# Kernel tuning notes

Measured on AMD Instinct MI355X. Metric: run time of the kernel, lower is better.

Reference implementation:

```python
import jax, jax.numpy as jnp
import numpy as np

B, S, D, H = 4, 1024, 2048, 16
DH = D // H  # 128
THETA = 10000.0


def setup_inputs() -> dict:
    key = jax.random.key(0)
    k1, k2, k3 = jax.random.split(key, 3)
    std_qkv = np.sqrt(2.0 / (D + 3 * D)).astype(np.float32)
    std_out = np.sqrt(2.0 / (D + D)).astype(np.float32)
    x = jax.random.normal(k1, (B, S, D), jnp.float32)
    w_qkv = jax.random.normal(k2, (D, 3 * D), jnp.float32) * std_qkv
    w_out = jax.random.normal(k3, (D, D), jnp.float32) * std_out
    # matrix-based RoPE table: [max_seq, d_head//2, 2, 2]
    freqs = jnp.arange(S, dtype=jnp.float32)[:, None] / THETA ** (
        2.0 * jnp.arange(DH // 2, dtype=jnp.float32) / DH)[None, :]
    eye = jnp.array([[1.0, 0.0], [0.0, 1.0]], jnp.float32)
    rot = jnp.array([[0.0, -1.0], [1.0, 0.0]], jnp.float32)
    rope_matrix = (jnp.cos(freqs)[:, :, None, None] * eye
                   + jnp.sin(freqs)[:, :, None, None] * rot)
    token_positions = jnp.arange(S, dtype=jnp.int32)
    return {"x": x, "w_qkv": w_qkv, "w_out": w_out,
            "rope_matrix": rope_matrix, "token_positions": token_positions}


def _apply_rope(t, pe):
    # t: [B, H, S, DH]; pe: [S, DH//2, 2, 2] (gathered by token_positions)
    tr = t.reshape(*t.shape[:-1], DH // 2, 2)  # interleaved (even, odd) pairs
    out = jnp.einsum('bhski,skoi->bhsko', tr, pe)
    return out.reshape(t.shape)


def reference(x, w_qkv, w_out, rope_matrix, token_positions):
    qkv = jnp.einsum('bsd,df->bsf', x, w_qkv)          # [B,S,3D]
    q, k, v = jnp.split(qkv, 3, axis=-1)
    to_heads = lambda t: t.reshape(B, S, H, DH).transpose(0, 2, 1, 3)
    q, k, v = to_heads(q), to_heads(k), to_heads(v)    # [B,H,S,DH]
    pe = rope_matrix[token_positions]                  # [S, DH//2, 2, 2]
    q = _apply_rope(q, pe)
    k = _apply_rope(k, pe)
    scores = jnp.einsum('bhqd,bhkd->bhqk', q, k) / np.float32(np.sqrt(DH))
    causal = jnp.tril(jnp.ones((S, S), dtype=bool))
    scores = jnp.where(causal, scores, -jnp.inf)
    attn = jax.nn.softmax(scores, axis=-1)
    ctx = jnp.einsum('bhqk,bhkd->bhqd', attn, v)       # [B,H,S,DH]
    ctx = ctx.transpose(0, 2, 1, 3).reshape(B, S, D)
    return jnp.einsum('bsd,df->bsf', ctx, w_out)
```

## Files before the change

kernel.cpp:

```cpp
#include <hip/hip_runtime.h>
#include <hip/hip_bf16.h>
#include <math.h>

#define Bn 4
#define Sn 1024
#define Dn 2048
#define Hn 16
#define DHn 128
#define BS (Bn * Sn)
#define QKVC (3 * Dn)

typedef __attribute__((ext_vector_type(8))) short short8;
typedef __attribute__((ext_vector_type(4))) float float4v;

__device__ inline unsigned short f2bf(float x) {
  union { float f; unsigned int u; } v; v.f = x;
  unsigned int r = v.u + 0x7fffu + ((v.u >> 16) & 1u);
  return (unsigned short)(r >> 16);
}
__device__ inline float bf2f(unsigned short b) {
  union { unsigned int u; float f; } v; v.u = ((unsigned int)b) << 16;
  return v.f;
}

__device__ __forceinline__ void gload16(const unsigned short* g, unsigned short* l) {
  __builtin_amdgcn_global_load_lds(
      (const __attribute__((address_space(1))) unsigned int*)g,
      (__attribute__((address_space(3))) unsigned int*)l, 16, 0, 0);
}

__global__ __launch_bounds__(256) void cvt_f32_bf16(
    const float* __restrict__ in, unsigned short* __restrict__ out, int n8) {
  int id = blockIdx.x * 256 + threadIdx.x;
  if (id >= n8) return;
  const float4* p = reinterpret_cast<const float4*>(in) + 2 * (size_t)id;
  float4 a = p[0], b = p[1];
  short8 o;
  o[0] = (short)f2bf(a.x); o[1] = (short)f2bf(a.y);
  o[2] = (short)f2bf(a.z); o[3] = (short)f2bf(a.w);
  o[4] = (short)f2bf(b.x); o[5] = (short)f2bf(b.y);
  o[6] = (short)f2bf(b.z); o[7] = (short)f2bf(b.w);
  *reinterpret_cast<short8*>(out + 8 * (size_t)id) = o;
}

__global__ __launch_bounds__(256) void transpose_cvt(
    const float* __restrict__ w, unsigned short* __restrict__ wT, int K, int N) {
  __shared__ unsigned short t[64][72];
  const int c0 = blockIdx.x * 64;
  const int r0 = blockIdx.y * 64;
  const int tid = threadIdx.x;
  const int r = tid >> 2;
  const int cb = (tid & 3) * 16;
#pragma unroll
  for (int it = 0; it < 4; ++it) {
    float4 v = *reinterpret_cast<const float4*>(&w[(long)(r0 + r) * N + c0 + cb + 4 * it]);
    t[r][cb + 4 * it + 0] = f2bf(v.x);
    t[r][cb + 4 * it + 1] = f2bf(v.y);
    t[r][cb + 4 * it + 2] = f2bf(v.z);
    t[r][cb + 4 * it + 3] = f2bf(v.w);
  }
  __syncthreads();
  unsigned short o[16];
#pragma unroll
  for (int e = 0; e < 16; ++e) o[e] = t[cb + e][r];
  unsigned short* dst = &wT[(long)(c0 + r) * K + r0 + cb];
  *reinterpret_cast<short8*>(dst) = *reinterpret_cast<short8*>(&o[0]);
  *reinterpret_cast<short8*>(dst + 8) = *reinterpret_cast<short8*>(&o[8]);
}

#define AB8(buf, h) ((buf) * 16384 + (h) * 8192)
#define BB8(buf) (32768 + (buf) * 8192)

#define VMW(n)                                                                 \
  asm volatile("s_waitcnt vmcnt(" #n ")" ::: "memory");                        \
  __builtin_amdgcn_sched_barrier(0);

#define PHASE(BUF, MIH, STAGE_STMT, WAIT_STMT)                                 \
  {                                                                            \
    __builtin_amdgcn_sched_barrier(0);                                         \
    short8 afr[2][2];                                                          \
    _Pragma("unroll") for (int mi2 = 0; mi2 < 2; ++mi2) {                      \
      const int mrow = wr * 64 + ((MIH) * 2 + mi2) * 16;                       \
      const int hh = mrow >> 7;                                                \
      const int rl = (mrow & 127) + c;                                         \
      _Pragma("unroll") for (int ks = 0; ks < 2; ++ks)                         \
        afr[mi2][ks] = *(const short8*)(lds + AB8(BUF, 0) + hh * 8192 +        \
            rl * 64 + (((ks * 4 + g) ^ cg7) << 3));                            \
    }                                                                          \
    if ((MIH) == 0) {                                                          \
      _Pragma("unroll") for (int ni = 0; ni < 4; ++ni)                         \
        _Pragma("unroll") for (int ks = 0; ks < 2; ++ks)                       \
          bfr[ni][ks] = *(const short8*)(lds + BB8(BUF) +                      \
              (wc * 64 + ni * 16 + c) * 64 + (((ks * 4 + g) ^ cg7) << 3));     \
    }                                                                          \
    STAGE_STMT;                                                                \
    __builtin_amdgcn_sched_barrier(0);                                         \
    __builtin_amdgcn_s_barrier();                                              \
    asm volatile("s_waitcnt lgkmcnt(0)" ::: "memory");                         \
    __builtin_amdgcn_sched_barrier(0);                                         \
    __builtin_amdgcn_s_setprio(1);                                             \
    _Pragma("unroll") for (int mi2 = 0; mi2 < 2; ++mi2)                        \
      _Pragma("unroll") for (int ni = 0; ni < 4; ++ni)                         \
        _Pragma("unroll") for (int ks = 0; ks < 2; ++ks)                       \
          acc[(MIH) * 2 + mi2][ni] = __builtin_amdgcn_mfma_f32_16x16x32_bf16(  \
              afr[mi2][ks], bfr[ni][ks], acc[(MIH) * 2 + mi2][ni], 0, 0, 0);   \
    __builtin_amdgcn_s_setprio(0);                                             \
    WAIT_STMT                                                                  \
    __builtin_amdgcn_s_barrier();                                              \
  }

#define GEMM_MAIN_LOOP(A_, BT_, K_)                                            \
  STAGE(A_ + (long)m0 * K_, AB8(0, 0));                                        \
  STAGE(A_ + (long)(m0 + 128) * K_, AB8(0, 1));                                \
  STAGE(BT_ + (long)n0 * K_, BB8(0));                                          \
  STAGE(BT_ + (long)n0 * K_ + 64, BB8(1));                                     \
  VMW(2)                                                                       \
  __builtin_amdgcn_s_barrier();                                                \
  for (int it2 = 0; it2 < nt / 2 - 1; ++it2) {                                 \
    const long T1 = (long)(2 * it2 + 1) * 64;                                  \
    const long T2 = (long)(2 * it2 + 2) * 64;                                  \
    const long T3 = (long)(2 * it2 + 3) * 64;                                  \
    PHASE(0, 0, STAGE(A_ + (long)m0 * K_ + T1, AB8(1, 0)), )                   \
    PHASE(0, 1,                                                                \
          { STAGE(A_ + (long)(m0 + 128) * K_ + T1, AB8(1, 1));                 \
            STAGE(BT_ + (long)n0 * K_ + T2, BB8(0)); }, VMW(2))                \
    PHASE(1, 0, STAGE(A_ + (long)m0 * K_ + T2, AB8(0, 0)), )                   \
    PHASE(1, 1,                                                                \
          { STAGE(A_ + (long)(m0 + 128) * K_ + T2, AB8(0, 1));                 \
            STAGE(BT_ + (long)n0 * K_ + T3, BB8(1)); }, VMW(2))                \
  }                                                                            \
  {                                                                            \
    const long TL = (long)(nt - 1) * 64;                                       \
    PHASE(0, 0, STAGE(A_ + (long)m0 * K_ + TL, AB8(1, 0)), )                   \
    PHASE(0, 1, STAGE(A_ + (long)(m0 + 128) * K_ + TL, AB8(1, 1)), VMW(0))     \
    PHASE(1, 0, {}, )                                                          \
    PHASE(1, 1, {}, )                                                          \
  }

__global__ __launch_bounds__(512, 2) void gemm_qkv(
    const unsigned short* __restrict__ A, const unsigned short* __restrict__ BT,
    const float* __restrict__ rope, const int* __restrict__ tpos,
    unsigned short* __restrict__ qR, unsigned short* __restrict__ kR,
    unsigned short* __restrict__ vT, int K) {
  __shared__ unsigned short lds[49152];
  const int tid = threadIdx.x;
  const int wid = tid >> 6, lane = tid & 63;
  const int c = lane & 15, g = lane >> 4;
  const int wr = wid >> 1, wc = wid & 1;
  const int cg7 = c & 7;

  const int nwg = gridDim.x * gridDim.y;
  const int bid = blockIdx.y * gridDim.x + blockIdx.x;
  const int swz = (bid & 7) * (nwg >> 3) + (bid >> 3);
  const int m0 = (swz % gridDim.x) * 256, n0 = (swz / gridDim.x) * 128;

  const int nt = K >> 6;

  float4v acc[4][4];
#pragma unroll
  for (int i = 0; i < 4; ++i)
#pragma unroll
    for (int j = 0; j < 4; ++j) acc[i][j] = (float4v){0.f, 0.f, 0.f, 0.f};
  short8 bfr[4][2];

  auto STAGE = [&](const unsigned short* gbase, int sbase) {
#pragma unroll
    for (int j = 0; j < 2; ++j) {
      const int ch = j * 512 + tid;
      const int r = ch >> 3;
      const int wo = (ch & 7) ^ (r & 7);
      gload16(gbase + (long)r * K + wo * 8, lds + sbase + j * 4096 + wid * 512);
    }
  };

  GEMM_MAIN_LOOP(A, BT, K)

  const int type = n0 >> 11;
  const int h = (n0 & 2047) >> 7;
  const long bh = (long)((m0 >> 10) * Hn + h);
  const int s0 = m0 & 1023;

  if (type == 2) {
#pragma unroll
    for (int mi = 0; mi < 4; ++mi)
#pragma unroll
      for (int ni = 0; ni < 4; ++ni)
#pragma unroll
        for (int j = 0; j < 4; ++j) {
          const int mm = wr * 64 + mi * 16 + g * 4 + j;
          const int nn = wc * 64 + ni * 16 + c;
          lds[nn * 264 + mm] = f2bf(acc[mi][ni][j]);
        }
    __syncthreads();
    unsigned short* dst = vT + bh * (long)DHn * Sn + s0;
#pragma unroll
    for (int it = 0; it < 8; ++it) {
      const int cid = it * 512 + tid;
      const int d = cid >> 5;
      const int sl = (cid & 31) * 8;
      short8 v = *reinterpret_cast<const short8*>(lds + d * 264 + sl);
      *reinterpret_cast<short8*>(dst + (long)d * Sn + sl) = v;
    }
  } else {
#pragma unroll
    for (int mi = 0; mi < 4; ++mi)
#pragma unroll
      for (int ni = 0; ni < 4; ++ni)
#pragma unroll
        for (int j = 0; j < 4; ++j) {
          const int mm = wr * 64 + mi * 16 + g * 4 + j;
          const int nn = wc * 64 + ni * 16 + c;
          lds[mm * 136 + nn] = f2bf(acc[mi][ni][j]);
        }
    __syncthreads();
    unsigned short* dst = (type == 0 ? qR : kR) + (bh * Sn + s0) * DHn;
    const float qsc = (type == 0) ? 0.1275174213f : 1.0f;
#pragma unroll
    for (int it = 0; it < 8; ++it) {
      const int cid = it * 512 + tid;
      const int r = cid >> 4;
      const int colc = (cid & 15) * 8;
      union { short8 v; unsigned short u[8]; } iw, ow;
      iw.v = *reinterpret_cast<const short8*>(lds + r * 136 + colc);
      const int pos = tpos[s0 + r];
      const float4* pe = reinterpret_cast<const float4*>(rope) +
                         (long)pos * 64 + (colc >> 1);
#pragma unroll
      for (int p = 0; p < 4; ++p) {
        const float4 m2 = pe[p];
        const float xx = bf2f(iw.u[2 * p]), yy = bf2f(iw.u[2 * p + 1]);
        ow.u[2 * p]     = f2bf((m2.x * xx + m2.y * yy) * qsc);
        ow.u[2 * p + 1] = f2bf((m2.z * xx + m2.w * yy) * qsc);
      }
      *reinterpret_cast<short8*>(dst + (long)r * DHn + colc) = ow.v;
    }
  }
}

__global__ __launch_bounds__(512, 2) void gemm_out(
    const unsigned short* __restrict__ A, const unsigned short* __restrict__ BT,
    float* __restrict__ Cout, int N, int K) {
  __shared__ unsigned short lds[49152];
  const int tid = threadIdx.x;
  const int wid = tid >> 6, lane = tid & 63;
  const int c = lane & 15, g = lane >> 4;
  const int wr = wid >> 1, wc = wid & 1;
  const int cg7 = c & 7;

  const int nwg = gridDim.x * gridDim.y;
  const int bid = blockIdx.y * gridDim.x + blockIdx.x;
  const int swz = (bid & 7) * (nwg >> 3) + (bid >> 3);
  const int m0 = (swz % gridDim.x) * 256, n0 = (swz / gridDim.x) * 128;

  const int nt = K >> 6;

  float4v acc[4][4];
#pragma unroll
  for (int i = 0; i < 4; ++i)
#pragma unroll
    for (int j = 0; j < 4; ++j) acc[i][j] = (float4v){0.f, 0.f, 0.f, 0.f};
  short8 bfr[4][2];

  auto STAGE = [&](const unsigned short* gbase, int sbase) {
#pragma unroll
    for (int j = 0; j < 2; ++j) {
      const int ch = j * 512 + tid;
      const int r = ch >> 3;
      const int wo = (ch & 7) ^ (r & 7);
      gload16(gbase + (long)r * K + wo * 8, lds + sbase + j * 4096 + wid * 512);
    }
  };

  GEMM_MAIN_LOOP(A, BT, K)

#pragma unroll
  for (int mi = 0; mi < 4; ++mi)
#pragma unroll
    for (int ni = 0; ni < 4; ++ni)
#pragma unroll
      for (int j = 0; j < 4; ++j) {
        const int m = m0 + wr * 64 + mi * 16 + g * 4 + j;
        const int n = n0 + wc * 64 + ni * 16 + c;
        Cout[(long)m * N + n] = acc[mi][ni][j];
      }
}
#undef PHASE
#undef GEMM_MAIN_LOOP

__global__ __launch_bounds__(256, 2) void attn_mfma(
    const unsigned short* __restrict__ qR, const unsigned short* __restrict__ kR,
    const unsigned short* __restrict__ vTd, unsigned short* __restrict__ ctx) {
  __shared__ unsigned short lds[32768];
  __shared__ unsigned short Ps[4][16][72];
  const int qt = gridDim.x - 1 - blockIdx.x;
  const int h = blockIdx.y, b = blockIdx.z;
  const int tid = threadIdx.x, wid = tid >> 6, lane = tid & 63;
  const int c = lane & 15, g = lane >> 4, cg7 = c & 7;
  const long bh = (long)(b * Hn + h);
  const unsigned short* kbase = kR + bh * Sn * DHn;
  const unsigned short* vbase = vTd + bh * DHn * Sn;

  short8 qf[4];
  {
    const unsigned short* qrow = qR + (bh * Sn + qt * 64 + wid * 16 + c) * DHn;
#pragma unroll
    for (int kc = 0; kc < 4; ++kc)
      qf[kc] = *reinterpret_cast<const short8*>(qrow + kc * 32 + g * 8);
  }

  auto STAGE = [&](int kt, int buf) {
#pragma unroll
    for (int j = 0; j < 4; ++j) {
      const int ch = j * 256 + tid;
      const int r = ch >> 4, wd = ch & 15;
      const int ws = (wd & 8) | ((wd & 7) ^ (r & 7));
      gload16(kbase + (long)kt * 8192 + r * 128 + ws * 8,
              lds + buf * 8192 + j * 2048 + wid * 512);
    }
#pragma unroll
    for (int j = 0; j < 4; ++j) {
      const int ch = j * 256 + tid;
      const int d = ch >> 3, sw = ch & 7;
      gload16(vbase + (long)d * Sn + kt * 64 + ((sw ^ (d & 7)) << 3),
              lds + 16384 + buf * 8192 + j * 2048 + wid * 512);
    }
  };

  float m = -INFINITY, lsum = 0.f;
  float4v ot[8];
#pragma unroll
  for (int fd = 0; fd < 8; ++fd) ot[fd] = (float4v){0.f, 0.f, 0.f, 0.f};

  STAGE(0, 0);
  __syncthreads();
  int cur = 0;

  for (int kt = 0; kt <= qt; ++kt) {
    if (kt < qt) STAGE(kt + 1, cur ^ 1);

    float4v scv[4];
#pragma unroll
    for (int f = 0; f < 4; ++f) scv[f] = (float4v){0.f, 0.f, 0.f, 0.f};
    __builtin_amdgcn_s_setprio(1);
#pragma unroll
    for (int f = 0; f < 4; ++f)
#pragma unroll
      for (int kc = 0; kc < 4; ++kc) {
        const int wp = kc * 4 + g;
        const int ws = (wp & 8) | ((wp & 7) ^ cg7);
        short8 kf = *reinterpret_cast<const short8*>(
            lds + cur * 8192 + (f * 16 + c) * 128 + ws * 8);
        scv[f] = __builtin_amdgcn_mfma_f32_16x16x32_bf16(kf, qf[kc], scv[f], 0, 0, 0);
      }
    __builtin_amdgcn_s_setprio(0);

    if (kt == qt) {
      const int qloc = wid * 16 + c;
#pragma unroll
      for (int f = 0; f < 4; ++f)
#pragma unroll
        for (int j = 0; j < 4; ++j)
          if (f * 16 + g * 4 + j > qloc) scv[f][j] = -INFINITY;
    }

    float tmax = -INFINITY;
#pragma unroll
    for (int f = 0; f < 4; ++f)
#pragma unroll
      for (int j = 0; j < 4; ++j) tmax = fmaxf(tmax, scv[f][j]);
    tmax = fmaxf(tmax, __shfl_xor(tmax, 16));
    tmax = fmaxf(tmax, __shfl_xor(tmax, 32));

    float mnew, corr;
    if (__all(tmax <= m + 8.f)) {
      mnew = m; corr = 1.f;
    } else {
      mnew = fmaxf(m, tmax);
      corr = exp2f(m - mnew);
#pragma unroll
      for (int fd = 0; fd < 8; ++fd) ot[fd] *= corr;
    }
    float psum = 0.f;
#pragma unroll
    for (int f = 0; f < 4; ++f)
#pragma unroll
      for (int j = 0; j < 4; ++j) {
        scv[f][j] = exp2f(scv[f][j] - mnew);
        psum += scv[f][j];
      }
    psum += __shfl_xor(psum, 16);
    psum += __shfl_xor(psum, 32);
    lsum = lsum * corr + psum;
    m = mnew;

#pragma unroll
    for (int f = 0; f < 4; ++f) {
      unsigned int lo = (unsigned)f2bf(scv[f][0]) | ((unsigned)f2bf(scv[f][1]) << 16);
      unsigned int hi = (unsigned)f2bf(scv[f][2]) | ((unsigned)f2bf(scv[f][3]) << 16);
      uint2 pk; pk.x = lo; pk.y = hi;
      *reinterpret_cast<uint2*>(&Ps[wid][c][f * 16 + g * 4]) = pk;
    }

    short8 pf0 = *reinterpret_cast<const short8*>(&Ps[wid][c][g * 8]);
    short8 pf1 = *reinterpret_cast<const short8*>(&Ps[wid][c][32 + g * 8]);
    __builtin_amdgcn_s_setprio(1);
#pragma unroll
    for (int fd = 0; fd < 8; ++fd) {
      short8 vf0 = *reinterpret_cast<const short8*>(
          lds + 16384 + cur * 8192 + (fd * 16 + c) * 64 + ((g ^ cg7) << 3));
      short8 vf1 = *reinterpret_cast<const short8*>(
          lds + 16384 + cur * 8192 + (fd * 16 + c) * 64 + (((g + 4) ^ cg7) << 3));
      ot[fd] = __builtin_amdgcn_mfma_f32_16x16x32_bf16(vf0, pf0, ot[fd], 0, 0, 0);
      ot[fd] = __builtin_amdgcn_mfma_f32_16x16x32_bf16(vf1, pf1, ot[fd], 0, 0, 0);
    }
    __builtin_amdgcn_s_setprio(0);

    __syncthreads();
    cur ^= 1;
  }

  const float inv = 1.0f / lsum;
  unsigned short* orow = ctx + (long)(b * Sn + qt * 64 + wid * 16 + c) * Dn + h * DHn;
#pragma unroll
  for (int fd = 0; fd < 8; ++fd) {
    const int d = fd * 16 + g * 4;
    uint2 pk;
    pk.x = (unsigned)f2bf(ot[fd][0] * inv) | ((unsigned)f2bf(ot[fd][1] * inv) << 16);
    pk.y = (unsigned)f2bf(ot[fd][2] * inv) | ((unsigned)f2bf(ot[fd][3] * inv) << 16);
    *reinterpret_cast<uint2*>(orow + d) = pk;
  }
}

extern "C" void kernel_launch(void* const* d_in, const int* in_sizes, int n_in,
                              void* d_out, int out_size, void* d_ws, size_t ws_size,
                              hipStream_t stream) {
  const float* x     = (const float*)d_in[0];
  const float* w_qkv = (const float*)d_in[1];
  const float* w_out = (const float*)d_in[2];
  const float* rope  = (const float*)d_in[3];
  const int*   tpos  = (const int*)d_in[4];
  float* out = (float*)d_out;

  unsigned short* x16    = (unsigned short*)d_ws;
  unsigned short* wqkvT  = x16 + (size_t)BS * Dn;
  unsigned short* woutT  = wqkvT + (size_t)Dn * QKVC;
  unsigned short* qR     = woutT + (size_t)Dn * Dn;
  unsigned short* kR     = qR + (size_t)BS * Dn;
  unsigned short* vT16   = kR + (size_t)BS * Dn;
  unsigned short* ctx16  = vT16 + (size_t)BS * Dn;

  cvt_f32_bf16<<<(BS * Dn / 8 + 255) / 256, 256, 0, stream>>>(x, x16, BS * Dn / 8);
  {
    dim3 g1(QKVC / 64, Dn / 64);
    transpose_cvt<<<g1, 256, 0, stream>>>(w_qkv, wqkvT, Dn, QKVC);
    dim3 g2(Dn / 64, Dn / 64);
    transpose_cvt<<<g2, 256, 0, stream>>>(w_out, woutT, Dn, Dn);
  }
  {
    dim3 grid(BS / 256, QKVC / 128);
    gemm_qkv<<<grid, 512, 0, stream>>>(x16, wqkvT, rope, tpos, qR, kR, vT16, Dn);
  }
  {
    dim3 grid(Sn / 64, Hn, Bn);
    attn_mfma<<<grid, 256, 0, stream>>>(qR, kR, vT16, ctx16);
  }
  {
    dim3 grid(BS / 256, Dn / 128);
    gemm_out<<<grid, 512, 0, stream>>>(ctx16, woutT, out, Dn, Dn);
  }
}
```

Measured before the change: 260.2 us.

## Process two query tiles per attention block to reuse staged K/V tiles

Each attention block now handles 128 query rows as two 64-row sub-tiles, keeping separate softmax state and output accumulators for each. Every staged K/V tile is consumed by both sub-tiles, which halves K/V global traffic and barrier count per query row. The grid is halved. The cost is doubled accumulator registers, which risks spills or lower occupancy, and fewer, longer blocks for the causal workload.

```diff
diff --git a/kernel.cpp b/kernel.cpp
--- a/kernel.cpp
+++ b/kernel.cpp
@@ -292,7 +292,7 @@
     const unsigned short* __restrict__ vTd, unsigned short* __restrict__ ctx) {
   __shared__ unsigned short lds[32768];
   __shared__ unsigned short Ps[4][16][72];
-  const int qt = gridDim.x - 1 - blockIdx.x;
+  const int qp = gridDim.x - 1 - blockIdx.x;
   const int h = blockIdx.y, b = blockIdx.z;
   const int tid = threadIdx.x, wid = tid >> 6, lane = tid & 63;
   const int c = lane & 15, g = lane >> 4, cg7 = c & 7;
@@ -300,12 +300,14 @@
   const unsigned short* kbase = kR + bh * Sn * DHn;
   const unsigned short* vbase = vTd + bh * DHn * Sn;
 
-  short8 qf[4];
-  {
-    const unsigned short* qrow = qR + (bh * Sn + qt * 64 + wid * 16 + c) * DHn;
+  short8 qf[2][4];
+#pragma unroll
+  for (int sub = 0; sub < 2; ++sub) {
+    const unsigned short* qrow =
+        qR + (bh * Sn + qp * 128 + sub * 64 + wid * 16 + c) * DHn;
 #pragma unroll
     for (int kc = 0; kc < 4; ++kc)
-      qf[kc] = *reinterpret_cast<const short8*>(qrow + kc * 32 + g * 8);
+      qf[sub][kc] = *reinterpret_cast<const short8*>(qrow + kc * 32 + g * 8);
   }
 
   auto STAGE = [&](int kt, int buf) {
@@ -326,108 +328,124 @@
     }
   };
 
-  float m = -INFINITY, lsum = 0.f;
-  float4v ot[8];
-#pragma unroll
-  for (int fd = 0; fd < 8; ++fd) ot[fd] = (float4v){0.f, 0.f, 0.f, 0.f};
-
+  float m[2] = {-INFINITY, -INFINITY}, lsum[2] = {0.f, 0.f};
+  float4v otA[8], otB[8];
+#pragma unroll
+  for (int fd = 0; fd < 8; ++fd) {
+    otA[fd] = (float4v){0.f, 0.f, 0.f, 0.f};
+    otB[fd] = (float4v){0.f, 0.f, 0.f, 0.f};
+  }
+
+  const int ntt = 2 * qp + 2;
   STAGE(0, 0);
   __syncthreads();
   int cur = 0;
 
-  for (int kt = 0; kt <= qt; ++kt) {
-    if (kt < qt) STAGE(kt + 1, cur ^ 1);
-
-    float4v scv[4];
-#pragma unroll
-    for (int f = 0; f < 4; ++f) scv[f] = (float4v){0.f, 0.f, 0.f, 0.f};
-    __builtin_amdgcn_s_setprio(1);
-#pragma unroll
-    for (int f = 0; f < 4; ++f)
-#pragma unroll
-      for (int kc = 0; kc < 4; ++kc) {
-        const int wp = kc * 4 + g;
-        const int ws = (wp & 8) | ((wp & 7) ^ cg7);
-        short8 kf = *reinterpret_cast<const short8*>(
-            lds + cur * 8192 + (f * 16 + c) * 128 + ws * 8);
-        scv[f] = __builtin_amdgcn_mfma_f32_16x16x32_bf16(kf, qf[kc], scv[f], 0, 0, 0);
-      }
-    __builtin_amdgcn_s_setprio(0);
-
-    if (kt == qt) {
-      const int qloc = wid * 16 + c;
+  for (int kt = 0; kt < ntt; ++kt) {
+    if (kt + 1 < ntt) STAGE(kt + 1, cur ^ 1);
+
+#pragma unroll
+    for (int sub = 0; sub < 2; ++sub) {
+      if (sub == 0 && kt == ntt - 1) continue;
+      float4v* ot = (sub == 0) ? otA : otB;
+
+      float4v scv[4];
+#pragma unroll
+      for (int f = 0; f < 4; ++f) scv[f] = (float4v){0.f, 0.f, 0.f, 0.f};
+      __builtin_amdgcn_s_setprio(1);
 #pragma unroll
       for (int f = 0; f < 4; ++f)
 #pragma unroll
-        for (int j = 0; j < 4; ++j)
-          if (f * 16 + g * 4 + j > qloc) scv[f][j] = -INFINITY;
-    }
-
-    float tmax = -INFINITY;
-#pragma unroll
-    for (int f = 0; f < 4; ++f)
-#pragma unroll
-      for (int j = 0; j < 4; ++j) tmax = fmaxf(tmax, scv[f][j]);
-    tmax = fmaxf(tmax, __shfl_xor(tmax, 16));
-    tmax = fmaxf(tmax, __shfl_xor(tmax, 32));
-
-    float mnew, corr;
-    if (__all(tmax <= m + 8.f)) {
-      mnew = m; corr = 1.f;
-    } else {
-      mnew = fmaxf(m, tmax);
-      corr = exp2f(m - mnew);
-#pragma unroll
-      for (int fd = 0; fd < 8; ++fd) ot[fd] *= corr;
-    }
-    float psum = 0.f;
-#pragma unroll
-    for (int f = 0; f < 4; ++f)
-#pragma unroll
-      for (int j = 0; j < 4; ++j) {
-        scv[f][j] = exp2f(scv[f][j] - mnew);
-        psum += scv[f][j];
-      }
-    psum += __shfl_xor(psum, 16);
-    psum += __shfl_xor(psum, 32);
-    lsum = lsum * corr + psum;
-    m = mnew;
-
-#pragma unroll
-    for (int f = 0; f < 4; ++f) {
-      unsigned int lo = (unsigned)f2bf(scv[f][0]) | ((unsigned)f2bf(scv[f][1]) << 16);
-      unsigned int hi = (unsigned)f2bf(scv[f][2]) | ((unsigned)f2bf(scv[f][3]) << 16);
-      uint2 pk; pk.x = lo; pk.y = hi;
-      *reinterpret_cast<uint2*>(&Ps[wid][c][f * 16 + g * 4]) = pk;
-    }
-
-    short8 pf0 = *reinterpret_cast<const short8*>(&Ps[wid][c][g * 8]);
-    short8 pf1 = *reinterpret_cast<const short8*>(&Ps[wid][c][32 + g * 8]);
-    __builtin_amdgcn_s_setprio(1);
-#pragma unroll
-    for (int fd = 0; fd < 8; ++fd) {
-      short8 vf0 = *reinterpret_cast<const short8*>(
-          lds + 16384 + cur * 8192 + (fd * 16 + c) * 64 + ((g ^ cg7) << 3));
-      short8 vf1 = *reinterpret_cast<const short8*>(
-          lds + 16384 + cur * 8192 + (fd * 16 + c) * 64 + (((g + 4) ^ cg7) << 3));
-      ot[fd] = __builtin_amdgcn_mfma_f32_16x16x32_bf16(vf0, pf0, ot[fd], 0, 0, 0);
-      ot[fd] = __builtin_amdgcn_mfma_f32_16x16x32_bf16(vf1, pf1, ot[fd], 0, 0, 0);
-    }
-    __builtin_amdgcn_s_setprio(0);
+        for (int kc = 0; kc < 4; ++kc) {
+          const int wp = kc * 4 + g;
+          const int ws = (wp & 8) | ((wp & 7) ^ cg7);
+          short8 kf = *reinterpret_cast<const short8*>(
+              lds + cur * 8192 + (f * 16 + c) * 128 + ws * 8);
+          scv[f] = __builtin_amdgcn_mfma_f32_16x16x32_bf16(kf, qf[sub][kc],
+                                                           scv[f], 0, 0, 0);
+        }
+      __builtin_amdgcn_s_setprio(0);
+
+      if (kt == 2 * qp + sub) {
+        const int qloc = wid * 16 + c;
+#pragma unroll
+        for (int f = 0; f < 4; ++f)
+#pragma unroll
+          for (int j = 0; j < 4; ++j)
+            if (f * 16 + g * 4 + j > qloc) scv[f][j] = -INFINITY;
+      }
+
+      float tmax = -INFINITY;
+#pragma unroll
+      for (int f = 0; f < 4; ++f)
+#pragma unroll
+        for (int j = 0; j < 4; ++j) tmax = fmaxf(tmax, scv[f][j]);
+      tmax = fmaxf(tmax, __shfl_xor(tmax, 16));
+      tmax = fmaxf(tmax, __shfl_xor(tmax, 32));
+
+      float mnew, corr;
+      if (__all(tmax <= m[sub] + 8.f)) {
+        mnew = m[sub]; corr = 1.f;
+      } else {
+        mnew = fmaxf(m[sub], tmax);
+        corr = exp2f(m[sub] - mnew);
+#pragma unroll
+        for (int fd = 0; fd < 8; ++fd) ot[fd] *= corr;
+      }
+      float psum = 0.f;
+#pragma unroll
+      for (int f = 0; f < 4; ++f)
+#pragma unroll
+        for (int j = 0; j < 4; ++j) {
+          scv[f][j] = exp2f(scv[f][j] - mnew);
+          psum += scv[f][j];
+        }
+      psum += __shfl_xor(psum, 16);
+      psum += __shfl_xor(psum, 32);
+      lsum[sub] = lsum[sub] * corr + psum;
+      m[sub] = mnew;
+
+#pragma unroll
+      for (int f = 0; f < 4; ++f) {
+        unsigned int lo = (unsigned)f2bf(scv[f][0]) | ((unsigned)f2bf(scv[f][1]) << 16);
+        unsigned int hi = (unsigned)f2bf(scv[f][2]) | ((unsigned)f2bf(scv[f][3]) << 16);
+        uint2 pk; pk.x = lo; pk.y = hi;
+        *reinterpret_cast<uint2*>(&Ps[wid][c][f * 16 + g * 4]) = pk;
+      }
+
+      short8 pf0 = *reinterpret_cast<const short8*>(&Ps[wid][c][g * 8]);
+      short8 pf1 = *reinterpret_cast<const short8*>(&Ps[wid][c][32 + g * 8]);
+      __builtin_amdgcn_s_setprio(1);
+#pragma unroll
+      for (int fd = 0; fd < 8; ++fd) {
+        short8 vf0 = *reinterpret_cast<const short8*>(
+            lds + 16384 + cur * 8192 + (fd * 16 + c) * 64 + ((g ^ cg7) << 3));
+        short8 vf1 = *reinterpret_cast<const short8*>(
+            lds + 16384 + cur * 8192 + (fd * 16 + c) * 64 + (((g + 4) ^ cg7) << 3));
+        ot[fd] = __builtin_amdgcn_mfma_f32_16x16x32_bf16(vf0, pf0, ot[fd], 0, 0, 0);
+        ot[fd] = __builtin_amdgcn_mfma_f32_16x16x32_bf16(vf1, pf1, ot[fd], 0, 0, 0);
+      }
+      __builtin_amdgcn_s_setprio(0);
+    }
 
     __syncthreads();
     cur ^= 1;
   }
 
-  const float inv = 1.0f / lsum;
-  unsigned short* orow = ctx + (long)(b * Sn + qt * 64 + wid * 16 + c) * Dn + h * DHn;
-#pragma unroll
-  for (int fd = 0; fd < 8; ++fd) {
-    const int d = fd * 16 + g * 4;
-    uint2 pk;
-    pk.x = (unsigned)f2bf(ot[fd][0] * inv) | ((unsigned)f2bf(ot[fd][1] * inv) << 16);
-    pk.y = (unsigned)f2bf(ot[fd][2] * inv) | ((unsigned)f2bf(ot[fd][3] * inv) << 16);
-    *reinterpret_cast<uint2*>(orow + d) = pk;
+#pragma unroll
+  for (int sub = 0; sub < 2; ++sub) {
+    const float4v* ot = (sub == 0) ? otA : otB;
+    const float inv = 1.0f / lsum[sub];
+    unsigned short* orow =
+        ctx + (long)(b * Sn + qp * 128 + sub * 64 + wid * 16 + c) * Dn + h * DHn;
+#pragma unroll
+    for (int fd = 0; fd < 8; ++fd) {
+      const int d = fd * 16 + g * 4;
+      uint2 pk;
+      pk.x = (unsigned)f2bf(ot[fd][0] * inv) | ((unsigned)f2bf(ot[fd][1] * inv) << 16);
+      pk.y = (unsigned)f2bf(ot[fd][2] * inv) | ((unsigned)f2bf(ot[fd][3] * inv) << 16);
+      *reinterpret_cast<uint2*>(orow + d) = pk;
+    }
   }
 }
 
@@ -461,7 +479,7 @@
     gemm_qkv<<<grid, 512, 0, stream>>>(x16, wqkvT, rope, tpos, qR, kR, vT16, Dn);
   }
   {
-    dim3 grid(Sn / 64, Hn, Bn);
+    dim3 grid(Sn / 128, Hn, Bn);
     attn_mfma<<<grid, 256, 0, stream>>>(qR, kR, vT16, ctx16);
   }
   {
```

Result: no change. 255.2 us (-1.9%).
